# Performance work log

Measured on AMD Instinct MI355X. Metric: run time of the kernel, lower is better.

## Reference

```python
import jax, jax.numpy as jnp
import numpy as np

B, S, D = 8, 1024, 1152
H = 16
HD = D // H
HID = int(D * 4.0)
LN_EPS = 1e-5


def layer_norm(x, w, b):
    m = jnp.mean(x, axis=-1, keepdims=True)
    v = jnp.mean(jnp.square(x - m), axis=-1, keepdims=True)
    return (x - m) * jax.lax.rsqrt(v + LN_EPS) * w + b


def modulate(x, shift, scale):
    # shift/scale: [B, D] broadcast over seq
    return x * (1.0 + scale[:, None, :]) + shift[:, None, :]


def setup_inputs() -> dict:
    key = jax.random.key(0)
    ks = jax.random.split(key, 16)
    s = 0.02
    return {
        "x": jax.random.normal(ks[0], (B, S, D), jnp.float32),
        "c": jax.random.normal(ks[1], (B, D), jnp.float32),
        "ln1_w": jnp.ones((D,), jnp.float32),
        "ln1_b": jnp.zeros((D,), jnp.float32),
        "wq": jax.random.normal(ks[2], (D, D), jnp.float32) * s,
        "wk": jax.random.normal(ks[3], (D, D), jnp.float32) * s,
        "wv": jax.random.normal(ks[4], (D, D), jnp.float32) * s,
        "wo": jax.random.normal(ks[5], (D, D), jnp.float32) * s,
        "wo_b": jnp.zeros((D,), jnp.float32),
        "ln2_w": jnp.ones((D,), jnp.float32),
        "ln2_b": jnp.zeros((D,), jnp.float32),
        "fc1_w": jax.random.normal(ks[6], (D, HID), jnp.float32) * s,
        "fc1_b": jnp.zeros((HID,), jnp.float32),
        "fc2_w": jax.random.normal(ks[7], (HID, D), jnp.float32) * s,
        "fc2_b": jnp.zeros((D,), jnp.float32),
        "ada_w": jax.random.normal(ks[8], (D, 6 * D), jnp.float32) * s,
        "ada_b": jnp.zeros((6 * D,), jnp.float32),
    }


def attention(x, wq, wk, wv, wo, wo_b):
    b, s, d = x.shape
    q = (x @ wq).reshape(b, s, H, HD).transpose(0, 2, 1, 3)  # [B,H,S,hd]
    k = (x @ wk).reshape(b, s, H, HD).transpose(0, 2, 1, 3)
    v = (x @ wv).reshape(b, s, H, HD).transpose(0, 2, 1, 3)
    scale = 1.0 / np.sqrt(HD).astype(np.float32)
    att = jnp.einsum("bhqd,bhkd->bhqk", q, k) * scale
    att = jax.nn.softmax(att, axis=-1)
    out = jnp.einsum("bhqk,bhkd->bhqd", att, v)
    out = out.transpose(0, 2, 1, 3).reshape(b, s, d)
    return out @ wo + wo_b


def reference(x, c, ln1_w, ln1_b, wq, wk, wv, wo, wo_b, ln2_w, ln2_b,
              fc1_w, fc1_b, fc2_w, fc2_b, ada_w, ada_b):
    mod = jax.nn.silu(c) @ ada_w + ada_b  # [B, 6D]
    sh_msa, sc_msa, g_msa, sh_mlp, sc_mlp, g_mlp = jnp.split(mod, 6, axis=1)
    h = modulate(layer_norm(x, ln1_w, ln1_b), sh_msa, sc_msa)
    x = x + g_msa[:, None, :] * attention(h, wq, wk, wv, wo, wo_b)
    h = modulate(layer_norm(x, ln2_w, ln2_b), sh_mlp, sc_mlp)
    h = jax.nn.gelu(h @ fc1_w + fc1_b, approximate=False) @ fc2_w + fc2_b
    x = x + g_mlp[:, None, :] * h
    return x
```

## Files before the change

kernel.cpp:

```cpp
#include <hip/hip_runtime.h>
#include <hip/hip_bf16.h>


typedef unsigned short u16;
typedef unsigned int u32;
typedef __attribute__((ext_vector_type(8))) short bf16x8;
typedef __attribute__((ext_vector_type(4))) float f32x4;
typedef __attribute__((ext_vector_type(16))) float f32x16;

#define MFMA16(a, b, c) __builtin_amdgcn_mfma_f32_16x16x32_bf16((a), (b), (c), 0, 0, 0)
#define MFMA32(a, b, c) __builtin_amdgcn_mfma_f32_32x32x16_bf16((a), (b), (c), 0, 0, 0)

__device__ __forceinline__ u16 f2bf(float f) {
  __hip_bfloat16 h = __float2bfloat16(f);
  return __builtin_bit_cast(u16, h);
}

__device__ __forceinline__ float bf2f(u16 u) {
  u32 v = ((u32)u) << 16;
  return __builtin_bit_cast(float, v);
}

__device__ __forceinline__ void gload16(const u16* g, u16* l) {
  __builtin_amdgcn_global_load_lds(
      (const __attribute__((address_space(1))) unsigned int*)(const void*)g,
      (__attribute__((address_space(3))) unsigned int*)(void*)l, 16, 0, 0);
}

__global__ __launch_bounds__(256) void k_modproj1(const float* __restrict__ cc,
                                                  const float* __restrict__ aw,
                                                  float* __restrict__ partial) {
  __shared__ float lc[8][144];
  int kc = blockIdx.y;
  for (int i = threadIdx.x; i < 1152; i += 256) {
    int b = i / 144, k = i % 144;
    float v = cc[b * 1152 + kc * 144 + k];
    lc[b][k] = v / (1.f + __expf(-v));
  }
  __syncthreads();
  int j = blockIdx.x * 256 + threadIdx.x;
  float acc[8] = {0, 0, 0, 0, 0, 0, 0, 0};
  for (int k = 0; k < 144; ++k) {
    float w = aw[(size_t)(kc * 144 + k) * 6912 + j];
    #pragma unroll
    for (int b = 0; b < 8; ++b) acc[b] += lc[b][k] * w;
  }
  #pragma unroll
  for (int b = 0; b < 8; ++b) partial[((size_t)kc * 8 + b) * 6912 + j] = acc[b];
}

__global__ __launch_bounds__(256) void k_modproj2(const float* __restrict__ partial,
                                                  const float* __restrict__ ab,
                                                  float* __restrict__ mo) {
  int j = blockIdx.x * 256 + threadIdx.x;
  float bias = ab[j];
  #pragma unroll
  for (int b = 0; b < 8; ++b) {
    float s = 0.f;
    #pragma unroll
    for (int kc = 0; kc < 8; ++kc) s += partial[((size_t)kc * 8 + b) * 6912 + j];
    mo[(size_t)b * 6912 + j] = s + bias;
  }
}

__global__ __launch_bounds__(256) void k_tcvt(const float* __restrict__ in, u16* __restrict__ out,
                                              int K, int N) {
  __shared__ float t[32][33];
  int tx = threadIdx.x & 31, ty = threadIdx.x >> 5;
  size_t bx = (size_t)blockIdx.x * 32, by = (size_t)blockIdx.y * 32;
  #pragma unroll
  for (int i = 0; i < 4; ++i) t[ty + 8 * i][tx] = in[(by + ty + 8 * i) * N + bx + tx];
  __syncthreads();
  #pragma unroll
  for (int i = 0; i < 4; ++i) out[(bx + ty + 8 * i) * K + by + tx] = f2bf(t[tx][ty + 8 * i]);
}

__global__ __launch_bounds__(256) void k_lnmod(const float* __restrict__ xin,
                                               const float* __restrict__ w,
                                               const float* __restrict__ bs,
                                               const float* __restrict__ mo,
                                               int sh_off, int sc_off, u16* __restrict__ o) {
  int row = blockIdx.x;
  int b = row >> 10;
  int tid = threadIdx.x;
  const float4* x4 = (const float4*)(xin + (size_t)row * 1152);
  float4 v0 = x4[tid];
  float4 v1 = make_float4(0.f, 0.f, 0.f, 0.f);
  if (tid < 32) v1 = x4[256 + tid];
  float s = v0.x + v0.y + v0.z + v0.w + v1.x + v1.y + v1.z + v1.w;
  float sq = v0.x * v0.x + v0.y * v0.y + v0.z * v0.z + v0.w * v0.w +
             v1.x * v1.x + v1.y * v1.y + v1.z * v1.z + v1.w * v1.w;
  #pragma unroll
  for (int d = 32; d > 0; d >>= 1) { s += __shfl_down(s, d); sq += __shfl_down(sq, d); }
  __shared__ float ps[4], pq[4];
  int wid = tid >> 6, lane = tid & 63;
  if (lane == 0) { ps[wid] = s; pq[wid] = sq; }
  __syncthreads();
  float S = ps[0] + ps[1] + ps[2] + ps[3];
  float SQ = pq[0] + pq[1] + pq[2] + pq[3];
  float mean = S * (1.f / 1152.f);
  float var = SQ * (1.f / 1152.f) - mean * mean;
  float rs = rsqrtf(var + 1e-5f);
  const float* shp = mo + (size_t)b * 6912 + sh_off;
  const float* scp = mo + (size_t)b * 6912 + sc_off;
  u16* orow = o + (size_t)row * 1152;
  {
    int col = 4 * tid;
    ushort4 u; float y;
    y = (v0.x - mean) * rs * w[col + 0] + bs[col + 0]; u.x = f2bf(y * (1.f + scp[col + 0]) + shp[col + 0]);
    y = (v0.y - mean) * rs * w[col + 1] + bs[col + 1]; u.y = f2bf(y * (1.f + scp[col + 1]) + shp[col + 1]);
    y = (v0.z - mean) * rs * w[col + 2] + bs[col + 2]; u.z = f2bf(y * (1.f + scp[col + 2]) + shp[col + 2]);
    y = (v0.w - mean) * rs * w[col + 3] + bs[col + 3]; u.w = f2bf(y * (1.f + scp[col + 3]) + shp[col + 3]);
    *(ushort4*)&orow[col] = u;
  }
  if (tid < 32) {
    int col = 1024 + 4 * tid;
    ushort4 u; float y;
    y = (v1.x - mean) * rs * w[col + 0] + bs[col + 0]; u.x = f2bf(y * (1.f + scp[col + 0]) + shp[col + 0]);
    y = (v1.y - mean) * rs * w[col + 1] + bs[col + 1]; u.y = f2bf(y * (1.f + scp[col + 1]) + shp[col + 1]);
    y = (v1.z - mean) * rs * w[col + 2] + bs[col + 2]; u.z = f2bf(y * (1.f + scp[col + 2]) + shp[col + 2]);
    y = (v1.w - mean) * rs * w[col + 3] + bs[col + 3]; u.w = f2bf(y * (1.f + scp[col + 3]) + shp[col + 3]);
    *(ushort4*)&orow[col] = u;
  }
}

template <int EPI>
__global__ __launch_bounds__(256) void k_gemm(const u16* __restrict__ A, const u16* __restrict__ Bt,
                                              int Kst, int klen, u16* __restrict__ Cb,
                                              float* __restrict__ Cf,
                                              const float* __restrict__ bias,
                                              const float* __restrict__ res,
                                              const float* __restrict__ mo, int goff,
                                              u16* __restrict__ vt) {
  const int tid = threadIdx.x;
  const int w = tid >> 6, lane = tid & 63;
  const int wr = w >> 1, wc = w & 1;
  const int l31 = lane & 31, hi = lane >> 5;

  const int nwg = gridDim.x * gridDim.y;
  const int id = blockIdx.y * gridDim.x + blockIdx.x;
  const int swz = (id & 7) * (nwg >> 3) + (id >> 3);
  const int tM = (swz / gridDim.x) * 128, tN = (swz % gridDim.x) * 128;
  const int N = gridDim.x * 128;
  const int koff = blockIdx.z * klen;

  __shared__ u16 lA[3][128 * 32];
  __shared__ u16 lB[3][128 * 32];
  f32x16 acc[2][2];
  #pragma unroll
  for (int m = 0; m < 2; ++m)
    #pragma unroll
    for (int n = 0; n < 2; ++n)
      #pragma unroll
      for (int r = 0; r < 16; ++r) acc[m][n][r] = 0.f;

  const int lrow = lane >> 2, lseg = lane & 3;
  const int fl = (lrow & 3) ^ ((lrow >> 2) & 3);
  const u16* gA = A + (size_t)(tM + w * 32 + lrow) * Kst + (lseg ^ fl) * 8 + koff;
  const u16* gB = Bt + (size_t)(tN + w * 32 + lrow) * Kst + (lseg ^ fl) * 8 + koff;
  const size_t rstep = (size_t)16 * Kst;
  const int wo0 = (w * 32) * 32, wo1 = (w * 32 + 16) * 32;
  const int fr = (l31 & 3) ^ ((l31 >> 2) & 3);
  const int c0 = (hi ^ fr) * 8;
  const int c1 = ((hi ^ fr) ^ 2) * 8;
  const int arow = (wr * 64 + l31) * 32;
  const int brow = (wc * 64 + l31) * 32;

#define STAGE(buf, ks)                        \
  do {                                        \
    gload16(gA + (ks), lA[buf] + wo0);        \
    gload16(gA + rstep + (ks), lA[buf] + wo1);\
    gload16(gB + (ks), lB[buf] + wo0);        \
    gload16(gB + rstep + (ks), lB[buf] + wo1);\
  } while (0)

#define COMPUTE(buf)                                                            \
  do {                                                                          \
    bf16x8 a00 = *(const bf16x8*)&lA[buf][arow + c0];                           \
    bf16x8 a01 = *(const bf16x8*)&lA[buf][arow + c1];                           \
    bf16x8 a10 = *(const bf16x8*)&lA[buf][arow + 1024 + c0];                    \
    bf16x8 a11 = *(const bf16x8*)&lA[buf][arow + 1024 + c1];                    \
    bf16x8 b00 = *(const bf16x8*)&lB[buf][brow + c0];                           \
    bf16x8 b01 = *(const bf16x8*)&lB[buf][brow + c1];                           \
    bf16x8 b10 = *(const bf16x8*)&lB[buf][brow + 1024 + c0];                    \
    bf16x8 b11 = *(const bf16x8*)&lB[buf][brow + 1024 + c1];                    \
    __builtin_amdgcn_s_setprio(1);                                              \
    acc[0][0] = MFMA32(a00, b00, acc[0][0]);                                    \
    acc[0][1] = MFMA32(a00, b10, acc[0][1]);                                    \
    acc[1][0] = MFMA32(a10, b00, acc[1][0]);                                    \
    acc[1][1] = MFMA32(a10, b10, acc[1][1]);                                    \
    acc[0][0] = MFMA32(a01, b01, acc[0][0]);                                    \
    acc[0][1] = MFMA32(a01, b11, acc[0][1]);                                    \
    acc[1][0] = MFMA32(a11, b01, acc[1][0]);                                    \
    acc[1][1] = MFMA32(a11, b11, acc[1][1]);                                    \
    __builtin_amdgcn_s_setprio(0);                                              \
  } while (0)

#define WAITBAR(Nst)                                          \
  do {                                                        \
    asm volatile("s_waitcnt vmcnt(" #Nst ")" ::: "memory");   \
    __builtin_amdgcn_s_barrier();                             \
    __builtin_amdgcn_sched_barrier(0);                        \
  } while (0)

  const int nt = klen >> 5;
  STAGE(0, 0);
  STAGE(1, 32);
  int ks = 64;
  for (int g = 0; g < nt / 3 - 1; ++g) {
    WAITBAR(4); STAGE(2, ks);      COMPUTE(0);
    WAITBAR(4); STAGE(0, ks + 32); COMPUTE(1);
    WAITBAR(4); STAGE(1, ks + 64); COMPUTE(2);
    ks += 96;
  }
  WAITBAR(4); STAGE(2, ks); COMPUTE(0);
  WAITBAR(4); COMPUTE(1);
  WAITBAR(0); COMPUTE(2);
#undef STAGE
#undef COMPUTE
#undef WAITBAR

  #pragma unroll
  for (int m = 0; m < 2; ++m)
    #pragma unroll
    for (int n = 0; n < 2; ++n) {
      int gcol = tN + wc * 64 + n * 32 + l31;
      #pragma unroll
      for (int q = 0; q < 4; ++q) {
        int grow0 = tM + wr * 64 + m * 32 + hi * 4 + q * 8;
        if (EPI == 3) {
          if (tN < 2304) {
            #pragma unroll
            for (int r = 0; r < 4; ++r)
              Cb[(size_t)(grow0 + r) * N + gcol] = f2bf(acc[m][n][q * 4 + r]);
          } else {
            int qq = gcol - 2304;
            int hh = qq / 72;
            int d = qq - hh * 72;
            int bb = grow0 >> 10, sl = grow0 & 1023;
            ushort4 u;
            u.x = f2bf(acc[m][n][q * 4 + 0]); u.y = f2bf(acc[m][n][q * 4 + 1]);
            u.z = f2bf(acc[m][n][q * 4 + 2]); u.w = f2bf(acc[m][n][q * 4 + 3]);
            *(ushort4*)&vt[(((size_t)bb * 16 + hh) * 72 + d) * 1024 + sl] = u;
          }
        } else if (EPI == 5) {
          u16* Po = Cb + (size_t)blockIdx.z * ((size_t)gridDim.y * 128) * N;
          #pragma unroll
          for (int r = 0; r < 4; ++r)
            Po[(size_t)(grow0 + r) * N + gcol] = f2bf(acc[m][n][q * 4 + r]);
        } else if (EPI == 1) {
          float g = mo[(size_t)(grow0 >> 10) * 6912 + goff + gcol];
          float bi = bias[gcol];
          #pragma unroll
          for (int r = 0; r < 4; ++r) {
            size_t idx = (size_t)(grow0 + r) * N + gcol;
            Cf[idx] = res[idx] + g * (acc[m][n][q * 4 + r] + bi);
          }
        } else {
          float bi = bias[gcol];
          #pragma unroll
          for (int r = 0; r < 4; ++r) {
            float z = acc[m][n][q * 4 + r] + bi;
            float z2 = z * z;
            float u = z * __fmaf_rn(z2, -0.0713548162f, -1.5957691216f);
            float e = __expf(u);
            Cb[(size_t)(grow0 + r) * N + gcol] = f2bf(z * __builtin_amdgcn_rcpf(1.f + e));
          }
        }
      }
    }
}

__global__ __launch_bounds__(256) void k_fc2red(const u16* __restrict__ p,
                                                const float* __restrict__ x1,
                                                const float* __restrict__ bias,
                                                const float* __restrict__ mo,
                                                float* __restrict__ out) {
  size_t i = ((size_t)blockIdx.x * 256 + threadIdx.x) * 4;
  int row = (int)(i / 1152);
  int col = (int)(i - (size_t)row * 1152);
  int b = row >> 10;
  ushort4 a0 = *(const ushort4*)(p + i);
  ushort4 a1 = *(const ushort4*)(p + 9437184ull + i);
  float4 r = *(const float4*)(x1 + i);
  const float* gp = mo + (size_t)b * 6912 + 5760 + col;
  const float* bp = bias + col;
  float4 o;
  o.x = r.x + gp[0] * (bf2f(a0.x) + bf2f(a1.x) + bp[0]);
  o.y = r.y + gp[1] * (bf2f(a0.y) + bf2f(a1.y) + bp[1]);
  o.z = r.z + gp[2] * (bf2f(a0.z) + bf2f(a1.z) + bp[2]);
  o.w = r.w + gp[3] * (bf2f(a0.w) + bf2f(a1.w) + bp[3]);
  *(float4*)(out + i) = o;
}

__global__ __launch_bounds__(256) void k_attn(const u16* __restrict__ QKV, const u16* __restrict__ Vt,
                                              u16* __restrict__ O) {
  const int tid = threadIdx.x;
  const int w = tid >> 6, lane = tid & 63;
  const int lr = lane & 15, kg = lane >> 4;
  int bx = blockIdx.x;
  bx = (bx & 7) * 256 + (bx >> 3);
  const int qt = bx & 15, h = (bx >> 4) & 15, b = bx >> 8;

  __shared__ u16 lQ[64][104];
  __shared__ u16 lK[64][104];
  __shared__ u16 lVt[80][72];
  __shared__ u16 lPt[4][16][72];

  const size_t qkbase = (size_t)b * 1024 * 3456 + (size_t)h * 72;
  const u16* Qg = QKV + qkbase;
  const u16* Kg = QKV + qkbase + 1152;
  const u16* Vg = Vt + ((size_t)(b * 16 + h) * 72) * 1024;

  const uint4 z4 = make_uint4(0, 0, 0, 0);
  for (int L = tid; L < 192; L += 256) {
    int r = L / 3, s = L - (L / 3) * 3;
    *(uint4*)&lQ[r][72 + s * 8] = z4;
    *(uint4*)&lK[r][72 + s * 8] = z4;
  }
  for (int L = tid; L < 72; L += 256) {
    int r = L / 9, s = L - (L / 9) * 9;
    *(uint4*)&lVt[72 + r][s * 8] = z4;
  }
  {
    int L = tid; int r = L / 9, s = L - r * 9;
    *(uint4*)&lQ[r][s * 8] = *(const uint4*)(Qg + (size_t)(qt * 64 + r) * 3456 + s * 8);
    L = tid + 256; r = L / 9; s = L - r * 9;
    *(uint4*)&lQ[r][s * 8] = *(const uint4*)(Qg + (size_t)(qt * 64 + r) * 3456 + s * 8);
    if (tid < 64) {
      L = tid + 512; r = L / 9; s = L - r * 9;
      *(uint4*)&lQ[r][s * 8] = *(const uint4*)(Qg + (size_t)(qt * 64 + r) * 3456 + s * 8);
    }
  }
  __syncthreads();

  bf16x8 bq[3];
  #pragma unroll
  for (int ks = 0; ks < 3; ++ks) bq[ks] = *(const bf16x8*)&lQ[w * 16 + lr][ks * 32 + kg * 8];

  const float scale = 0.11785113019775793f;
  float mrun = -1e30f, lrun = 0.f;
  f32x4 oacc[5];
  #pragma unroll
  for (int nd = 0; nd < 5; ++nd) oacc[nd] = f32x4{0.f, 0.f, 0.f, 0.f};

  for (int kt = 0; kt < 16; ++kt) {
    __syncthreads();
    {
      int L = tid; int r = L / 9, s = L - (L / 9) * 9;
      *(uint4*)&lK[r][s * 8] = *(const uint4*)(Kg + (size_t)(kt * 64 + r) * 3456 + s * 8);
      int d = tid >> 3, sg = tid & 7;
      *(uint4*)&lVt[d][sg * 8] = *(const uint4*)(Vg + (size_t)d * 1024 + kt * 64 + sg * 8);
      L = tid + 256; r = L / 9; s = L - r * 9;
      *(uint4*)&lK[r][s * 8] = *(const uint4*)(Kg + (size_t)(kt * 64 + r) * 3456 + s * 8);
      d = (tid + 256) >> 3; sg = tid & 7;
      *(uint4*)&lVt[d][sg * 8] = *(const uint4*)(Vg + (size_t)d * 1024 + kt * 64 + sg * 8);
      if (tid < 64) {
        L = tid + 512; r = L / 9; s = L - r * 9;
        *(uint4*)&lK[r][s * 8] = *(const uint4*)(Kg + (size_t)(kt * 64 + r) * 3456 + s * 8);
        d = (tid + 512) >> 3;
        *(uint4*)&lVt[d][sg * 8] = *(const uint4*)(Vg + (size_t)d * 1024 + kt * 64 + sg * 8);
      }
    }
    __syncthreads();

    f32x4 sfr[4];
    __builtin_amdgcn_s_setprio(1);
    #pragma unroll
    for (int kb = 0; kb < 4; ++kb) {
      f32x4 sv = f32x4{0.f, 0.f, 0.f, 0.f};
      #pragma unroll
      for (int ks = 0; ks < 3; ++ks) {
        bf16x8 ak = *(const bf16x8*)&lK[kb * 16 + lr][ks * 32 + kg * 8];
        sv = MFMA16(ak, bq[ks], sv);
      }
      sfr[kb] = sv;
    }
    __builtin_amdgcn_s_setprio(0);

    float mx = sfr[0][0];
    #pragma unroll
    for (int kb = 0; kb < 4; ++kb)
      #pragma unroll
      for (int r = 0; r < 4; ++r) mx = fmaxf(mx, sfr[kb][r]);
    mx = fmaxf(mx, __shfl_xor(mx, 16));
    mx = fmaxf(mx, __shfl_xor(mx, 32));
    mx *= scale;
    float mn = fmaxf(mrun, mx);
    float al = __expf(mrun - mn);
    mrun = mn;
    float sum = 0.f;
    #pragma unroll
    for (int kb = 0; kb < 4; ++kb) {
      #pragma unroll
      for (int rp = 0; rp < 2; ++rp) {
        float p0 = __expf(__fmaf_rn(sfr[kb][2 * rp], scale, -mn));
        float p1 = __expf(__fmaf_rn(sfr[kb][2 * rp + 1], scale, -mn));
        sum += p0 + p1;
        u32 pk = (u32)f2bf(p0) | ((u32)f2bf(p1) << 16);
        *(u32*)&lPt[w][lr][kb * 16 + kg * 4 + rp * 2] = pk;
      }
    }
    sum += __shfl_xor(sum, 16);
    sum += __shfl_xor(sum, 32);
    lrun = lrun * al + sum;
    #pragma unroll
    for (int nd = 0; nd < 5; ++nd)
      #pragma unroll
      for (int r = 0; r < 4; ++r) oacc[nd][r] *= al;

    __builtin_amdgcn_s_setprio(1);
    #pragma unroll
    for (int s = 0; s < 2; ++s) {
      bf16x8 bp = *(const bf16x8*)&lPt[w][lr][s * 32 + kg * 8];
      #pragma unroll
      for (int nd = 0; nd < 5; ++nd) {
        bf16x8 av = *(const bf16x8*)&lVt[nd * 16 + lr][s * 32 + kg * 8];
        oacc[nd] = MFMA16(av, bp, oacc[nd]);
      }
    }
    __builtin_amdgcn_s_setprio(0);
  }

  float inv = 1.f / lrun;
  size_t orow = ((size_t)b * 1024 + qt * 64 + w * 16 + lr) * 1152 + h * 72;
  #pragma unroll
  for (int nd = 0; nd < 5; ++nd) {
    int d0 = nd * 16 + kg * 4;
    if (d0 < 72) {
      ushort4 u;
      u.x = f2bf(oacc[nd][0] * inv);
      u.y = f2bf(oacc[nd][1] * inv);
      u.z = f2bf(oacc[nd][2] * inv);
      u.w = f2bf(oacc[nd][3] * inv);
      *(ushort4*)&O[orow + d0] = u;
    }
  }
}

extern "C" void kernel_launch(void* const* d_in, const int* in_sizes, int n_in,
                              void* d_out, int out_size, void* d_ws, size_t ws_size,
                              hipStream_t stream) {
  const float* x     = (const float*)d_in[0];
  const float* c     = (const float*)d_in[1];
  const float* ln1_w = (const float*)d_in[2];
  const float* ln1_b = (const float*)d_in[3];
  const float* wq    = (const float*)d_in[4];
  const float* wk    = (const float*)d_in[5];
  const float* wv    = (const float*)d_in[6];
  const float* wo    = (const float*)d_in[7];
  const float* wo_b  = (const float*)d_in[8];
  const float* ln2_w = (const float*)d_in[9];
  const float* ln2_b = (const float*)d_in[10];
  const float* fc1_w = (const float*)d_in[11];
  const float* fc1_b = (const float*)d_in[12];
  const float* fc2_w = (const float*)d_in[13];
  const float* fc2_b = (const float*)d_in[14];
  const float* ada_w = (const float*)d_in[15];
  const float* ada_b = (const float*)d_in[16];
  float* out = (float*)d_out;

  char* base = (char*)d_ws;
  size_t off = 0;
  auto alloc = [&](size_t nbytes) -> void* {
    void* p = base + off;
    off += (nbytes + 255) & ~(size_t)255;
    return p;
  };
  const size_t MD = 8192ull * 1152;
  float* partial = (float*)alloc(64ull * 6912 * 4);
  float* modb   = (float*)alloc(55296 * 4);
  u16* qkvT = (u16*)alloc(3456ull * 1152 * 2);
  u16* woT  = (u16*)alloc(1152ull * 1152 * 2);
  u16* fc1T = (u16*)alloc(4608ull * 1152 * 2);
  u16* fc2T = (u16*)alloc(1152ull * 4608 * 2);
  u16* hbuf = (u16*)alloc(MD * 2);
  float* x1 = (float*)alloc(MD * 4);
  u16* vtb  = (u16*)alloc(128ull * 72 * 1024 * 2);
  u16* fc2p = (u16*)alloc(2ull * MD * 2);
  u16* big  = (u16*)alloc(8192ull * 4608 * 2);
  u16* qkv = big;
  u16* m1 = big;

  k_modproj1<<<dim3(27, 8), 256, 0, stream>>>(c, ada_w, partial);
  k_modproj2<<<27, 256, 0, stream>>>(partial, ada_b, modb);
  k_tcvt<<<dim3(36, 36), 256, 0, stream>>>(wq, qkvT, 1152, 1152);
  k_tcvt<<<dim3(36, 36), 256, 0, stream>>>(wk, qkvT + 1152ull * 1152, 1152, 1152);
  k_tcvt<<<dim3(36, 36), 256, 0, stream>>>(wv, qkvT + 2304ull * 1152, 1152, 1152);
  k_tcvt<<<dim3(36, 36), 256, 0, stream>>>(wo, woT, 1152, 1152);
  k_tcvt<<<dim3(144, 36), 256, 0, stream>>>(fc1_w, fc1T, 1152, 4608);
  k_tcvt<<<dim3(36, 144), 256, 0, stream>>>(fc2_w, fc2T, 4608, 1152);

  k_lnmod<<<8192, 256, 0, stream>>>(x, ln1_w, ln1_b, modb, 0, 1152, hbuf);
  k_gemm<3><<<dim3(27, 64), 256, 0, stream>>>(hbuf, qkvT, 1152, 1152, qkv, nullptr, nullptr, nullptr, nullptr, 0, vtb);
  k_attn<<<2048, 256, 0, stream>>>(qkv, vtb, hbuf);
  k_gemm<1><<<dim3(9, 64), 256, 0, stream>>>(hbuf, woT, 1152, 1152, nullptr, x1, wo_b, x, modb, 2304, nullptr);
  k_lnmod<<<8192, 256, 0, stream>>>(x1, ln2_w, ln2_b, modb, 3456, 4608, hbuf);
  k_gemm<2><<<dim3(36, 64), 256, 0, stream>>>(hbuf, fc1T, 1152, 1152, m1, nullptr, fc1_b, nullptr, nullptr, 0, nullptr);
  k_gemm<5><<<dim3(9, 64, 2), 256, 0, stream>>>(m1, fc2T, 4608, 2304, fc2p, nullptr, nullptr, nullptr, nullptr, 0, nullptr);
  k_fc2red<<<9216, 256, 0, stream>>>(fc2p, x1, fc2_b, modb, out);
}
```

Baseline: 581.3 us.

## Add 256x256-tile 8-wave GEMM kernel for QKV and FC1 projections

Introduces a new GEMM kernel with 512 threads and 256x256 output tiles (each wave computes 128x64) and uses it for the QKV and FC1 GEMMs. Larger tiles raise arithmetic intensity and cut redundant global/LDS loads of A and B per FLOP. The QKV grid now covers 3584 columns, so the weight buffer is enlarged to 3584 rows and out-of-range columns are masked in the epilogue. The padded rows of that buffer are never written, so the masked tile wastes some compute, and the bigger accumulator set raises register pressure.

```diff
diff --git a/kernel.cpp b/kernel.cpp
--- a/kernel.cpp
+++ b/kernel.cpp
@@ -125,6 +125,142 @@
 }
 
 template <int EPI>
+__global__ __launch_bounds__(512, 2) void k_gemm8(const u16* __restrict__ A,
+                                                  const u16* __restrict__ Bt,
+                                                  int Kst, int klen,
+                                                  u16* __restrict__ Cb,
+                                                  const float* __restrict__ bias,
+                                                  u16* __restrict__ vt) {
+  const int tid = threadIdx.x;
+  const int w = tid >> 6, lane = tid & 63;
+  const int wm = w >> 2, wn = w & 3;
+  const int l31 = lane & 31, hi = lane >> 5;
+
+  const int nwg = gridDim.x * gridDim.y;
+  const int id = blockIdx.y * gridDim.x + blockIdx.x;
+  const int swz = (id & 7) * (nwg >> 3) + (id >> 3);
+  const int tM = (swz / gridDim.x) * 256, tN = (swz % gridDim.x) * 256;
+  const int koff = 0;
+
+  __shared__ u16 lA[3][256 * 32];
+  __shared__ u16 lB[3][256 * 32];
+  f32x16 acc[4][2];
+  #pragma unroll
+  for (int m = 0; m < 4; ++m)
+    #pragma unroll
+    for (int n = 0; n < 2; ++n)
+      #pragma unroll
+      for (int r = 0; r < 16; ++r) acc[m][n][r] = 0.f;
+
+  const int lrow = lane >> 2, lseg = lane & 3;
+  const int fl = (lrow & 3) ^ ((lrow >> 2) & 3);
+  const u16* gA = A + (size_t)(tM + w * 32 + lrow) * Kst + (lseg ^ fl) * 8 + koff;
+  const u16* gB = Bt + (size_t)(tN + w * 32 + lrow) * Kst + (lseg ^ fl) * 8 + koff;
+  const size_t rstep = (size_t)16 * Kst;
+  const int wo0 = (w * 32) * 32, wo1 = (w * 32 + 16) * 32;
+  const int fr = (l31 & 3) ^ ((l31 >> 2) & 3);
+  const int c0 = (hi ^ fr) * 8;
+  const int c1 = ((hi ^ fr) ^ 2) * 8;
+  const int arow = (wm * 128 + l31) * 32;
+  const int brow = (wn * 64 + l31) * 32;
+
+#define STAGE(buf, ks)                        \
+  do {                                        \
+    gload16(gA + (ks), lA[buf] + wo0);        \
+    gload16(gA + rstep + (ks), lA[buf] + wo1);\
+    gload16(gB + (ks), lB[buf] + wo0);        \
+    gload16(gB + rstep + (ks), lB[buf] + wo1);\
+  } while (0)
+
+#define COMPUTE(buf)                                                              \
+  do {                                                                            \
+    bf16x8 af[4][2], bf[2][2];                                                    \
+    _Pragma("unroll")                                                             \
+    for (int m = 0; m < 4; ++m) {                                                 \
+      af[m][0] = *(const bf16x8*)&lA[buf][arow + m * 1024 + c0];                  \
+      af[m][1] = *(const bf16x8*)&lA[buf][arow + m * 1024 + c1];                  \
+    }                                                                             \
+    _Pragma("unroll")                                                             \
+    for (int n = 0; n < 2; ++n) {                                                 \
+      bf[n][0] = *(const bf16x8*)&lB[buf][brow + n * 1024 + c0];                  \
+      bf[n][1] = *(const bf16x8*)&lB[buf][brow + n * 1024 + c1];                  \
+    }                                                                             \
+    __builtin_amdgcn_s_setprio(1);                                                \
+    _Pragma("unroll")                                                             \
+    for (int m = 0; m < 4; ++m)                                                   \
+      _Pragma("unroll")                                                           \
+      for (int n = 0; n < 2; ++n) acc[m][n] = MFMA32(af[m][0], bf[n][0], acc[m][n]); \
+    _Pragma("unroll")                                                             \
+    for (int m = 0; m < 4; ++m)                                                   \
+      _Pragma("unroll")                                                           \
+      for (int n = 0; n < 2; ++n) acc[m][n] = MFMA32(af[m][1], bf[n][1], acc[m][n]); \
+    __builtin_amdgcn_s_setprio(0);                                                \
+  } while (0)
+
+#define WAITBAR(Nst)                                          \
+  do {                                                        \
+    asm volatile("s_waitcnt vmcnt(" #Nst ")" ::: "memory");   \
+    __builtin_amdgcn_s_barrier();                             \
+    __builtin_amdgcn_sched_barrier(0);                        \
+  } while (0)
+
+  const int nt = klen >> 5;
+  STAGE(0, 0);
+  STAGE(1, 32);
+  int ks = 64;
+  for (int g = 0; g < nt / 3 - 1; ++g) {
+    WAITBAR(4); STAGE(2, ks);      COMPUTE(0);
+    WAITBAR(4); STAGE(0, ks + 32); COMPUTE(1);
+    WAITBAR(4); STAGE(1, ks + 64); COMPUTE(2);
+    ks += 96;
+  }
+  WAITBAR(4); STAGE(2, ks); COMPUTE(0);
+  WAITBAR(4); COMPUTE(1);
+  WAITBAR(0); COMPUTE(2);
+#undef STAGE
+#undef COMPUTE
+#undef WAITBAR
+
+  #pragma unroll
+  for (int m = 0; m < 4; ++m)
+    #pragma unroll
+    for (int n = 0; n < 2; ++n) {
+      int gcol = tN + wn * 64 + n * 32 + l31;
+      #pragma unroll
+      for (int q = 0; q < 4; ++q) {
+        int grow0 = tM + wm * 128 + m * 32 + hi * 4 + q * 8;
+        if (EPI == 3) {
+          if (gcol < 2304) {
+            #pragma unroll
+            for (int r = 0; r < 4; ++r)
+              Cb[(size_t)(grow0 + r) * 3456 + gcol] = f2bf(acc[m][n][q * 4 + r]);
+          } else if (gcol < 3456) {
+            int qq = gcol - 2304;
+            int hh = qq / 72;
+            int d = qq - hh * 72;
+            int bb = grow0 >> 10, sl = grow0 & 1023;
+            ushort4 u;
+            u.x = f2bf(acc[m][n][q * 4 + 0]); u.y = f2bf(acc[m][n][q * 4 + 1]);
+            u.z = f2bf(acc[m][n][q * 4 + 2]); u.w = f2bf(acc[m][n][q * 4 + 3]);
+            *(ushort4*)&vt[(((size_t)bb * 16 + hh) * 72 + d) * 1024 + sl] = u;
+          }
+        } else {
+          const int NC = gridDim.x * 256;
+          float bi = bias[gcol];
+          #pragma unroll
+          for (int r = 0; r < 4; ++r) {
+            float z = acc[m][n][q * 4 + r] + bi;
+            float z2 = z * z;
+            float u = z * __fmaf_rn(z2, -0.0713548162f, -1.5957691216f);
+            float e = __expf(u);
+            Cb[(size_t)(grow0 + r) * NC + gcol] = f2bf(z * __builtin_amdgcn_rcpf(1.f + e));
+          }
+        }
+      }
+    }
+}
+
+template <int EPI>
 __global__ __launch_bounds__(256) void k_gemm(const u16* __restrict__ A, const u16* __restrict__ Bt,
                                               int Kst, int klen, u16* __restrict__ Cb,
                                               float* __restrict__ Cf,
@@ -228,43 +364,18 @@
       #pragma unroll
       for (int q = 0; q < 4; ++q) {
         int grow0 = tM + wr * 64 + m * 32 + hi * 4 + q * 8;
-        if (EPI == 3) {
-          if (tN < 2304) {
-            #pragma unroll
-            for (int r = 0; r < 4; ++r)
-              Cb[(size_t)(grow0 + r) * N + gcol] = f2bf(acc[m][n][q * 4 + r]);
-          } else {
-            int qq = gcol - 2304;
-            int hh = qq / 72;
-            int d = qq - hh * 72;
-            int bb = grow0 >> 10, sl = grow0 & 1023;
-            ushort4 u;
-            u.x = f2bf(acc[m][n][q * 4 + 0]); u.y = f2bf(acc[m][n][q * 4 + 1]);
-            u.z = f2bf(acc[m][n][q * 4 + 2]); u.w = f2bf(acc[m][n][q * 4 + 3]);
-            *(ushort4*)&vt[(((size_t)bb * 16 + hh) * 72 + d) * 1024 + sl] = u;
-          }
-        } else if (EPI == 5) {
+        if (EPI == 5) {
           u16* Po = Cb + (size_t)blockIdx.z * ((size_t)gridDim.y * 128) * N;
           #pragma unroll
           for (int r = 0; r < 4; ++r)
             Po[(size_t)(grow0 + r) * N + gcol] = f2bf(acc[m][n][q * 4 + r]);
-        } else if (EPI == 1) {
+        } else {
           float g = mo[(size_t)(grow0 >> 10) * 6912 + goff + gcol];
           float bi = bias[gcol];
           #pragma unroll
           for (int r = 0; r < 4; ++r) {
             size_t idx = (size_t)(grow0 + r) * N + gcol;
             Cf[idx] = res[idx] + g * (acc[m][n][q * 4 + r] + bi);
-          }
-        } else {
-          float bi = bias[gcol];
-          #pragma unroll
-          for (int r = 0; r < 4; ++r) {
-            float z = acc[m][n][q * 4 + r] + bi;
-            float z2 = z * z;
-            float u = z * __fmaf_rn(z2, -0.0713548162f, -1.5957691216f);
-            float e = __expf(u);
-            Cb[(size_t)(grow0 + r) * N + gcol] = f2bf(z * __builtin_amdgcn_rcpf(1.f + e));
           }
         }
       }
@@ -470,7 +581,7 @@
   const size_t MD = 8192ull * 1152;
   float* partial = (float*)alloc(64ull * 6912 * 4);
   float* modb   = (float*)alloc(55296 * 4);
-  u16* qkvT = (u16*)alloc(3456ull * 1152 * 2);
+  u16* qkvT = (u16*)alloc(3584ull * 1152 * 2);
   u16* woT  = (u16*)alloc(1152ull * 1152 * 2);
   u16* fc1T = (u16*)alloc(4608ull * 1152 * 2);
   u16* fc2T = (u16*)alloc(1152ull * 4608 * 2);
@@ -492,11 +603,11 @@
   k_tcvt<<<dim3(36, 144), 256, 0, stream>>>(fc2_w, fc2T, 4608, 1152);
 
   k_lnmod<<<8192, 256, 0, stream>>>(x, ln1_w, ln1_b, modb, 0, 1152, hbuf);
-  k_gemm<3><<<dim3(27, 64), 256, 0, stream>>>(hbuf, qkvT, 1152, 1152, qkv, nullptr, nullptr, nullptr, nullptr, 0, vtb);
+  k_gemm8<3><<<dim3(14, 32), 512, 0, stream>>>(hbuf, qkvT, 1152, 1152, qkv, nullptr, vtb);
   k_attn<<<2048, 256, 0, stream>>>(qkv, vtb, hbuf);
   k_gemm<1><<<dim3(9, 64), 256, 0, stream>>>(hbuf, woT, 1152, 1152, nullptr, x1, wo_b, x, modb, 2304, nullptr);
   k_lnmod<<<8192, 256, 0, stream>>>(x1, ln2_w, ln2_b, modb, 3456, 4608, hbuf);
-  k_gemm<2><<<dim3(36, 64), 256, 0, stream>>>(hbuf, fc1T, 1152, 1152, m1, nullptr, fc1_b, nullptr, nullptr, 0, nullptr);
+  k_gemm8<2><<<dim3(18, 32), 512, 0, stream>>>(hbuf, fc1T, 1152, 1152, m1, fc1_b, nullptr);
   k_gemm<5><<<dim3(9, 64, 2), 256, 0, stream>>>(m1, fc2T, 4608, 2304, fc2p, nullptr, nullptr, nullptr, nullptr, 0, nullptr);
   k_fc2red<<<9216, 256, 0, stream>>>(fc2p, x1, fc2_b, modb, out);
 }
```

Result: no change. 577.3 us (-0.7%).
